# Optimization experiments

Hardware: AMD Instinct MI355X
Metric: run time of the kernel (lower is better)

Reference implementation:

```python
import jax, jax.numpy as jnp
import numpy as np

N = 100_000      # nodes
D = 64           # in_dim
E = 1_600_000    # edges (avg degree 16)
P_L = 0.5        # leaky slope for low-pass gate
P_H = 0.5        # leaky slope for high-pass gate


def setup_inputs() -> dict:
    key = jax.random.key(0)
    ks = jax.random.split(key, 10)
    h = jax.random.normal(ks[0], (N, D), jnp.float32)
    d = jax.random.uniform(ks[1], (N,), jnp.float32)  # degree norms 1/sqrt(deg)
    src = jax.random.randint(ks[2], (E,), 0, N)
    dst = jax.random.randint(ks[3], (E,), 0, N)
    # xavier_normal(gain=1.414) scale ~ gain*sqrt(2/(fan_in+fan_out))
    sg = 1.414 * np.sqrt(2.0 / (2 * D + 1))
    sr = 1.414 * np.sqrt(2.0 / (2 * D + D))
    Wl = jax.random.normal(ks[4], (1, 2 * D), jnp.float32) * sg
    bl = jnp.zeros((1,), jnp.float32)
    Wh = jax.random.normal(ks[5], (1, 2 * D), jnp.float32) * sg
    bh = jnp.zeros((1,), jnp.float32)
    Wr = jax.random.normal(ks[6], (D, 2 * D), jnp.float32) * sr
    br = jnp.zeros((D,), jnp.float32)
    return {"h": h, "d": d, "src": src, "dst": dst,
            "Wl": Wl, "bl": bl, "Wh": Wh, "bh": bh, "Wr": Wr, "br": br}


def reference(h, d, src, dst, Wl, bl, Wh, bh, Wr, br):
    # gate_x(cat([h_dst, h_src])) == h_dst @ W[:, :D] + h_src @ W[:, D:] + b
    # -> project once per node [N], gather per edge [E] (avoids [E,2D] concat)
    low_dst = h @ Wl[0, :D]
    low_src = h @ Wl[0, D:]
    _low = low_dst[dst] + low_src[src] + bl[0]                     # [E]
    g_low = jnp.tanh(jax.nn.relu(jnp.where(_low > 0, _low, -P_L * _low)))

    high_dst = h @ Wh[0, :D]
    high_src = h @ Wh[0, D:]
    _high = high_dst[dst] + high_src[src] + bh[0]                  # [E]
    g_high = jnp.tanh(-jax.nn.relu(jnp.where(_high > 0, _high, -P_H * _high)))

    dd = d[dst] * d[src]                                           # [E]
    e_low = g_low * dd
    e_high = g_high * dd

    h_src = h[src]                                                 # [E, D]
    z_low = jax.ops.segment_sum(h_src * e_low[:, None], dst, num_segments=N)
    z_high = jax.ops.segment_sum(h_src * e_high[:, None], dst, num_segments=N)

    z = jnp.concatenate([z_low, z_high], axis=1)                   # [N, 2D]
    return z @ Wr.T + br                                           # [N, D]
```

## Files before the change

kernel.cpp:

```cpp
#include <hip/hip_runtime.h>
#include <hip/hip_fp16.h>
#include <math.h>

#define N_NODES 100000
#define D_DIM   64
#define N_EDGES 1600000
#define P_L 0.5f
#define P_H 0.5f

#define NPB   32
#define NB    3125
#define TILE  2048
#define NT    784
#define GRP   28
#define GT    28
#define CAP   768
#define ZS    132


typedef unsigned int uint;
typedef unsigned short ushort_t;
typedef float f2 __attribute__((ext_vector_type(2)));

__device__ inline ushort_t f2bf(float f) {
    uint u = __float_as_uint(f);
    uint r = (u + 0x7fffu + ((u >> 16) & 1u)) >> 16;
    return (ushort_t)r;
}

__device__ inline float tanh_pos(float x) {
    return 1.f - 2.f / (__expf(2.f * x) + 1.f);
}

__device__ inline void fma16(uint gy, uint4 hv, f2* acc) {
    float el = __half2float(__ushort_as_half((unsigned short)(gy & 0xffffu)));
    float eh = __half2float(__ushort_as_half((unsigned short)(gy >> 16)));
    f2 f01 = {__uint_as_float(hv.x << 16), __uint_as_float(hv.x & 0xffff0000u)};
    f2 f23 = {__uint_as_float(hv.y << 16), __uint_as_float(hv.y & 0xffff0000u)};
    f2 f45 = {__uint_as_float(hv.z << 16), __uint_as_float(hv.z & 0xffff0000u)};
    f2 f67 = {__uint_as_float(hv.w << 16), __uint_as_float(hv.w & 0xffff0000u)};
    acc[0] += f01 * el; acc[1] += f23 * el; acc[2] += f45 * el; acc[3] += f67 * el;
    acc[4] += f01 * eh; acc[5] += f23 * eh; acc[6] += f45 * eh; acc[7] += f67 * eh;
}

__device__ inline unsigned long long match_dl(int dl, bool active) {
    unsigned long long m = __ballot(active);
    #pragma unroll
    for (int b = 0; b < 5; ++b) {
        unsigned long long bal = __ballot(active && ((dl >> b) & 1));
        m &= ((dl >> b) & 1) ? bal : ~bal;
    }
    return m;
}

__global__ __launch_bounds__(256) void node_gates_kernel(
    const float* __restrict__ h, const float* __restrict__ dvec,
    const float* __restrict__ Wl, const float* __restrict__ Wh,
    ushort_t* __restrict__ hbf,
    float4* __restrict__ gdst4, float4* __restrict__ gsrc4)
{
    int tid = threadIdx.x;
    int lane = tid & 63;
    int half = lane >> 5;
    int l32 = lane & 31;
    int node = blockIdx.x * 8 + (tid >> 6) * 2 + half;

    float2 hv2 = *(const float2*)(h + (size_t)node * 64 + l32 * 2);
    uint pk = (uint)f2bf(hv2.x) | ((uint)f2bf(hv2.y) << 16);
    ((uint*)hbf)[(size_t)node * 32 + l32] = pk;

    float pld = hv2.x * Wl[2 * l32]      + hv2.y * Wl[2 * l32 + 1];
    float pls = hv2.x * Wl[64 + 2 * l32] + hv2.y * Wl[64 + 2 * l32 + 1];
    float phd = hv2.x * Wh[2 * l32]      + hv2.y * Wh[2 * l32 + 1];
    float phs = hv2.x * Wh[64 + 2 * l32] + hv2.y * Wh[64 + 2 * l32 + 1];
    #pragma unroll
    for (int m = 16; m >= 1; m >>= 1) {
        pld += __shfl_xor(pld, m);
        pls += __shfl_xor(pls, m);
        phd += __shfl_xor(phd, m);
        phs += __shfl_xor(phs, m);
    }
    if (l32 == 0) {
        float d = dvec[node];
        gdst4[node] = make_float4(pld, phd, d, 0.f);
        gsrc4[node] = make_float4(pls, phs, d, 0.f);
    }
}

__global__ __launch_bounds__(512) void bucket_hist_kernel(const int* __restrict__ dst,
                                                          int* __restrict__ T) {
    __shared__ int hist[NB];
    int tid = threadIdx.x;
    for (int i = tid; i < NB; i += 512) hist[i] = 0;
    __syncthreads();
    int base = blockIdx.x * TILE;
    #pragma unroll
    for (int j = 0; j < TILE / 512; ++j) {
        int e = base + j * 512 + tid;
        if (e < N_EDGES) atomicAdd(&hist[dst[e] >> 5], 1);
    }
    __syncthreads();
    int* row = T + (size_t)blockIdx.x * NB;
    for (int i = tid; i < NB; i += 512) row[i] = hist[i];
}

__global__ __launch_bounds__(1024) void scanA1_kernel(int* __restrict__ T,
                                                      int* __restrict__ S) {
    int b = blockIdx.x * 1024 + threadIdx.x;
    if (b >= NB) return;
    int g = blockIdx.y;
    int run = 0;
    #pragma unroll
    for (int w = g * GT; w < g * GT + GT; ++w) {
        int idx = w * NB + b;
        int v = T[idx];
        T[idx] = run;
        run += v;
    }
    S[(size_t)g * NB + b] = run;
}

__global__ __launch_bounds__(1024) void scanA2_kernel(int* __restrict__ S,
                                                      int* __restrict__ totG) {
    int b = blockIdx.x * 1024 + threadIdx.x;
    if (b >= NB) return;
    int run = 0;
    #pragma unroll
    for (int g = 0; g < GRP; ++g) {
        int idx = g * NB + b;
        int v = S[idx];
        S[idx] = run;
        run += v;
    }
    totG[b] = run;
}

__global__ __launch_bounds__(1024) void scanB_kernel(const int* __restrict__ totG,
                                                     int* __restrict__ baseG,
                                                     int* __restrict__ bucketoffs,
                                                     const float* __restrict__ Wr,
                                                     float* __restrict__ wrt) {
    int tid = threadIdx.x;
    for (int idx = tid; idx < 64 * 128; idx += 1024) {
        int c = idx >> 7;
        int k = idx & 127;
        wrt[k * 64 + c] = Wr[idx];
    }

    __shared__ int scan_lds[1024];
    int a[4];
    int s = 0;
    #pragma unroll
    for (int i = 0; i < 4; ++i) {
        int b = tid * 4 + i;
        a[i] = (b < NB) ? totG[b] : 0;
        s += a[i];
    }
    scan_lds[tid] = s;
    __syncthreads();
    for (int d = 1; d < 1024; d <<= 1) {
        int v = (tid >= d) ? scan_lds[tid - d] : 0;
        __syncthreads();
        scan_lds[tid] += v;
        __syncthreads();
    }
    int excl = scan_lds[tid] - s;
    int total = scan_lds[1023];
    #pragma unroll
    for (int i = 0; i < 4; ++i) {
        int b = tid * 4 + i;
        if (b < NB) { baseG[b] = excl; bucketoffs[b] = excl; }
        excl += a[i];
    }
    if (tid == 0) bucketoffs[NB] = total;
}

__global__ __launch_bounds__(512) void place_kernel(
    const int* __restrict__ src, const int* __restrict__ dst,
    const int* __restrict__ T, const int* __restrict__ S,
    const int* __restrict__ baseG,
    const float4* __restrict__ gdst4, const float4* __restrict__ gsrc4,
    const float* __restrict__ bl, const float* __restrict__ bh,
    uint2* __restrict__ ebuf)
{
    __shared__ int cur[NB];
    int tid = threadIdx.x;
    const int* row  = T + (size_t)blockIdx.x * NB;
    const int* Srow = S + (size_t)(blockIdx.x / GT) * NB;
    for (int i = tid; i < NB; i += 512) cur[i] = row[i] + Srow[i] + baseG[i];
    __syncthreads();

    float bl0 = bl[0], bh0 = bh[0];
    int base = blockIdx.x * TILE;
    #pragma unroll
    for (int j = 0; j < TILE / 512; ++j) {
        int e = base + j * 512 + tid;
        if (e >= N_EDGES) continue;
        int t = dst[e];
        int s = src[e];
        float4 gt = gdst4[t];
        float4 gs = gsrc4[s];
        float xl = gt.x + gs.x + bl0;
        float xh = gt.y + gs.y + bh0;
        float ll = xl > 0.f ? xl : -P_L * xl;
        float hh = xh > 0.f ? xh : -P_H * xh;
        float dd = gt.z * gs.z;
        float el =  tanh_pos(ll) * dd;
        float eh = -tanh_pos(hh) * dd;
        uint ge = (uint)__half_as_ushort(__float2half_rn(el))
                | ((uint)__half_as_ushort(__float2half_rn(eh)) << 16);
        int b  = t >> 5;
        uint dl = (uint)(t & 31);
        int pos = atomicAdd(&cur[b], 1);
        ebuf[pos] = make_uint2((uint)s | (dl << 17), ge);
    }
}

__global__ __launch_bounds__(512) void accum_final_kernel(
    const int* __restrict__ bucketoffs, const uint2* __restrict__ ebuf,
    const ushort_t* __restrict__ hbf, const float* __restrict__ wrt,
    const float* __restrict__ br, float* __restrict__ out)
{
    __shared__ float z[NPB * ZS];
    __shared__ uint2 srec[CAP];
    __shared__ int ncount[NPB];
    __shared__ int nbase[NPB];
    __shared__ int ncur[NPB];

    int tid = threadIdx.x;
    int lane = tid & 63;
    int bk = blockIdx.x;
    int beg = bucketoffs[bk];
    int end = bucketoffs[bk + 1];
    int cnt = end - beg;
    if (cnt > CAP) cnt = CAP;

    if (tid < NPB) ncount[tid] = 0;

    bool hA = tid < cnt;
    bool hB = tid + 512 < cnt;
    uint2 rA = hA ? ebuf[beg + tid] : make_uint2(0, 0);
    uint2 rB = hB ? ebuf[beg + tid + 512] : make_uint2(0, 0);

    {
        const uint* pa = (const uint*)(hbf + (size_t)(rA.x & 0x1FFFF) * 64);
        const uint* pb = (const uint*)(hbf + (size_t)(rB.x & 0x1FFFF) * 64);
        uint p0 = hA ? pa[0]  : 0u;
        uint p1 = hA ? pa[16] : 0u;
        uint p2 = hB ? pb[0]  : 0u;
        uint p3 = hB ? pb[16] : 0u;
        asm volatile("" :: "v"(p0), "v"(p1), "v"(p2), "v"(p3));
    }
    __syncthreads();

    int dlA = (int)((rA.x >> 17) & 31u);
    int dlB = (int)((rB.x >> 17) & 31u);

    unsigned long long mA = match_dl(dlA, hA);
    if (hA && lane == (int)__builtin_ctzll(mA))
        atomicAdd(&ncount[dlA], (int)__popcll(mA));
    unsigned long long mB = match_dl(dlB, hB);
    if (hB && lane == (int)__builtin_ctzll(mB))
        atomicAdd(&ncount[dlB], (int)__popcll(mB));
    __syncthreads();

    if (tid < 32) {
        int v = ncount[tid];
        int p = v;
        #pragma unroll
        for (int d = 1; d < 32; d <<= 1) {
            int x = __shfl_up(p, d);
            if (tid >= d) p += x;
        }
        nbase[tid] = p - v;
        ncur[tid]  = p - v;
    }
    __syncthreads();

    if (hA) {
        int ldr = (int)__builtin_ctzll(mA);
        int base = 0;
        if (lane == ldr) base = atomicAdd(&ncur[dlA], (int)__popcll(mA));
        base = __shfl(base, ldr);
        int rank = (int)__popcll(mA & ((1ull << lane) - 1ull));
        srec[base + rank] = rA;
    }
    if (hB) {
        int ldr = (int)__builtin_ctzll(mB);
        int base = 0;
        if (lane == ldr) base = atomicAdd(&ncur[dlB], (int)__popcll(mB));
        base = __shfl(base, ldr);
        int rank = (int)__popcll(mB & ((1ull << lane) - 1ull));
        srec[base + rank] = rB;
    }
    __syncthreads();

    int sg = tid >> 3;
    int l8 = tid & 7;
    int node4 = sg >> 1;
    int par = sg & 1;
    int rbeg = nbase[node4];
    int rend = ncur[node4];

    f2 acc[8];
    #pragma unroll
    for (int j = 0; j < 8; ++j) acc[j] = (f2){0.f, 0.f};

    int k = rbeg + par;
    for (; k + 6 < rend; k += 8) {
        uint2 r0 = srec[k];
        uint2 r1 = srec[k + 2];
        uint2 r2 = srec[k + 4];
        uint2 r3 = srec[k + 6];
        uint4 h0 = *(const uint4*)(hbf + (size_t)(r0.x & 0x1FFFF) * 64 + l8 * 8);
        uint4 h1 = *(const uint4*)(hbf + (size_t)(r1.x & 0x1FFFF) * 64 + l8 * 8);
        uint4 h2 = *(const uint4*)(hbf + (size_t)(r2.x & 0x1FFFF) * 64 + l8 * 8);
        uint4 h3 = *(const uint4*)(hbf + (size_t)(r3.x & 0x1FFFF) * 64 + l8 * 8);
        fma16(r0.y, h0, acc);
        fma16(r1.y, h1, acc);
        fma16(r2.y, h2, acc);
        fma16(r3.y, h3, acc);
    }
    for (; k < rend; k += 2) {
        uint2 r0 = srec[k];
        uint4 hv = *(const uint4*)(hbf + (size_t)(r0.x & 0x1FFFF) * 64 + l8 * 8);
        fma16(r0.y, hv, acc);
    }

    float* zp = &z[node4 * ZS + l8 * 8];
    if (par == 0) {
        *(float4*)(zp + 0)  = make_float4(acc[0].x, acc[0].y, acc[1].x, acc[1].y);
        *(float4*)(zp + 4)  = make_float4(acc[2].x, acc[2].y, acc[3].x, acc[3].y);
        *(float4*)(zp + 64) = make_float4(acc[4].x, acc[4].y, acc[5].x, acc[5].y);
        *(float4*)(zp + 68) = make_float4(acc[6].x, acc[6].y, acc[7].x, acc[7].y);
    }
    __syncthreads();
    if (par == 1) {
        float4 z0 = *(float4*)(zp + 0);
        float4 z1 = *(float4*)(zp + 4);
        float4 z2 = *(float4*)(zp + 64);
        float4 z3 = *(float4*)(zp + 68);
        *(float4*)(zp + 0)  = make_float4(z0.x + acc[0].x, z0.y + acc[0].y, z0.z + acc[1].x, z0.w + acc[1].y);
        *(float4*)(zp + 4)  = make_float4(z1.x + acc[2].x, z1.y + acc[2].y, z1.z + acc[3].x, z1.w + acc[3].y);
        *(float4*)(zp + 64) = make_float4(z2.x + acc[4].x, z2.y + acc[4].y, z2.z + acc[5].x, z2.w + acc[5].y);
        *(float4*)(zp + 68) = make_float4(z3.x + acc[6].x, z3.y + acc[6].y, z3.z + acc[7].x, z3.w + acc[7].y);
    }
    __syncthreads();

    int node = tid >> 4;
    int g = tid & 15;
    f2 fa0 = {0.f, 0.f}, fa1 = {0.f, 0.f};
    const float* zrow = z + node * ZS;
    #pragma unroll 2
    for (int kk = 0; kk < 128; kk += 4) {
        float4 z4 = *(const float4*)(zrow + kk);
        const float* wp = wrt + kk * 64 + g * 4;
        float4 w0 = *(const float4*)(wp);
        float4 w1 = *(const float4*)(wp + 64);
        float4 w2 = *(const float4*)(wp + 128);
        float4 w3 = *(const float4*)(wp + 192);
        fa0 += (f2){w0.x, w0.y} * z4.x; fa1 += (f2){w0.z, w0.w} * z4.x;
        fa0 += (f2){w1.x, w1.y} * z4.y; fa1 += (f2){w1.z, w1.w} * z4.y;
        fa0 += (f2){w2.x, w2.y} * z4.z; fa1 += (f2){w2.z, w2.w} * z4.z;
        fa0 += (f2){w3.x, w3.y} * z4.w; fa1 += (f2){w3.z, w3.w} * z4.w;
    }
    int n = bk * NPB + node;
    float* op = out + (size_t)n * 64 + g * 4;
    const float* bp = br + g * 4;
    *(float4*)(op) = make_float4(fa0.x + bp[0], fa0.y + bp[1], fa1.x + bp[2], fa1.y + bp[3]);
}

extern "C" void kernel_launch(void* const* d_in, const int* in_sizes, int n_in,
                              void* d_out, int out_size, void* d_ws, size_t ws_size,
                              hipStream_t stream) {
    const float* h    = (const float*)d_in[0];
    const float* dvec = (const float*)d_in[1];
    const int*   src  = (const int*)  d_in[2];
    const int*   dst  = (const int*)  d_in[3];
    const float* Wl   = (const float*)d_in[4];
    const float* bl   = (const float*)d_in[5];
    const float* Wh   = (const float*)d_in[6];
    const float* bh   = (const float*)d_in[7];
    const float* Wr   = (const float*)d_in[8];
    const float* br   = (const float*)d_in[9];
    float* out = (float*)d_out;

    char* ws = (char*)d_ws;
    size_t off = 0;
    auto alloc = [&](size_t bytes) { char* p = ws + off; off += (bytes + 255) & ~size_t(255); return p; };

    ushort_t* hbf       = (ushort_t*)alloc((size_t)N_NODES * 64 * 2);
    float4*   gdst4     = (float4*)  alloc((size_t)N_NODES * 16);
    float4*   gsrc4     = (float4*)  alloc((size_t)N_NODES * 16);
    float*    wrt       = (float*)   alloc(64 * 128 * 4);
    int*      T         = (int*)     alloc((size_t)NT * NB * 4);
    int*      S         = (int*)     alloc((size_t)GRP * NB * 4);
    int*      totG      = (int*)     alloc((size_t)NB * 4);
    int*      baseG     = (int*)     alloc((size_t)NB * 4);
    int*      bucketoffs= (int*)     alloc((size_t)(NB + 1) * 4);
    uint2*    ebuf      = (uint2*)   alloc((size_t)N_EDGES * 8);

    node_gates_kernel<<<N_NODES / 8, 256, 0, stream>>>(h, dvec, Wl, Wh, hbf, gdst4, gsrc4);
    bucket_hist_kernel<<<NT, 512, 0, stream>>>(dst, T);
    {
        dim3 g1((NB + 1023) / 1024, GRP);
        scanA1_kernel<<<g1, 1024, 0, stream>>>(T, S);
    }
    scanA2_kernel<<<(NB + 1023) / 1024, 1024, 0, stream>>>(S, totG);
    scanB_kernel<<<1, 1024, 0, stream>>>(totG, baseG, bucketoffs, Wr, wrt);
    place_kernel<<<NT, 512, 0, stream>>>(src, dst, T, S, baseG, gdst4, gsrc4, bl, bh, ebuf);
    accum_final_kernel<<<NB, 512, 0, stream>>>(bucketoffs, ebuf, hbf, wrt, br, out);
}
```

Measured before the change: 305.9 us.

## Split each accumulation bucket across two 256-thread blocks by node half

The accumulation kernel now launches two 256-thread blocks per 32-node bucket. Each block reads the whole bucket's edge records but keeps only those whose destination falls in its 16-node half, then sorts, accumulates and projects just those nodes. The aim is more, smaller blocks with less shared memory each, which should help occupancy and load balance. In exchange every bucket's records are read twice, the hbf prefetch touch is dropped, and a new CAPH cap of 512 records per half could truncate edges if a half-bucket holds more.

```diff
diff --git a/kernel.cpp b/kernel.cpp
--- a/kernel.cpp
+++ b/kernel.cpp
@@ -14,7 +14,8 @@
 #define NT    784
 #define GRP   28
 #define GT    28
-#define CAP   768
+#define CAPB  768
+#define CAPH  512
 #define ZS    132
 
 
@@ -43,10 +44,10 @@
     acc[4] += f01 * eh; acc[5] += f23 * eh; acc[6] += f45 * eh; acc[7] += f67 * eh;
 }
 
-__device__ inline unsigned long long match_dl(int dl, bool active) {
+__device__ inline unsigned long long match4(int dl, bool active) {
     unsigned long long m = __ballot(active);
     #pragma unroll
-    for (int b = 0; b < 5; ++b) {
+    for (int b = 0; b < 4; ++b) {
         unsigned long long bal = __ballot(active && ((dl >> b) & 1));
         m &= ((dl >> b) & 1) ? bal : ~bal;
     }
@@ -216,59 +217,60 @@
     }
 }
 
-__global__ __launch_bounds__(512) void accum_final_kernel(
+__global__ __launch_bounds__(256) void accum_final_kernel(
     const int* __restrict__ bucketoffs, const uint2* __restrict__ ebuf,
     const ushort_t* __restrict__ hbf, const float* __restrict__ wrt,
     const float* __restrict__ br, float* __restrict__ out)
 {
-    __shared__ float z[NPB * ZS];
-    __shared__ uint2 srec[CAP];
-    __shared__ int ncount[NPB];
-    __shared__ int nbase[NPB];
-    __shared__ int ncur[NPB];
+    __shared__ float z[16 * ZS];
+    __shared__ uint2 srec[CAPH];
+    __shared__ int ncount[16];
+    __shared__ int nbase[16];
+    __shared__ int ncur[16];
 
     int tid = threadIdx.x;
     int lane = tid & 63;
-    int bk = blockIdx.x;
+    int bk = blockIdx.x >> 1;
+    int hf = blockIdx.x & 1;
     int beg = bucketoffs[bk];
     int end = bucketoffs[bk + 1];
     int cnt = end - beg;
-    if (cnt > CAP) cnt = CAP;
-
-    if (tid < NPB) ncount[tid] = 0;
+    if (cnt > CAPB) cnt = CAPB;
+
+    if (tid < 16) ncount[tid] = 0;
 
     bool hA = tid < cnt;
-    bool hB = tid + 512 < cnt;
-    uint2 rA = hA ? ebuf[beg + tid] : make_uint2(0, 0);
-    uint2 rB = hB ? ebuf[beg + tid + 512] : make_uint2(0, 0);
-
-    {
-        const uint* pa = (const uint*)(hbf + (size_t)(rA.x & 0x1FFFF) * 64);
-        const uint* pb = (const uint*)(hbf + (size_t)(rB.x & 0x1FFFF) * 64);
-        uint p0 = hA ? pa[0]  : 0u;
-        uint p1 = hA ? pa[16] : 0u;
-        uint p2 = hB ? pb[0]  : 0u;
-        uint p3 = hB ? pb[16] : 0u;
-        asm volatile("" :: "v"(p0), "v"(p1), "v"(p2), "v"(p3));
-    }
-    __syncthreads();
-
-    int dlA = (int)((rA.x >> 17) & 31u);
-    int dlB = (int)((rB.x >> 17) & 31u);
-
-    unsigned long long mA = match_dl(dlA, hA);
-    if (hA && lane == (int)__builtin_ctzll(mA))
+    bool hB = tid + 256 < cnt;
+    bool hC = tid + 512 < cnt;
+    uint2 rA = hA ? ebuf[beg + tid]       : make_uint2(0, 0);
+    uint2 rB = hB ? ebuf[beg + tid + 256] : make_uint2(0, 0);
+    uint2 rC = hC ? ebuf[beg + tid + 512] : make_uint2(0, 0);
+    __syncthreads();
+
+    int dA5 = (int)((rA.x >> 17) & 31u);
+    int dB5 = (int)((rB.x >> 17) & 31u);
+    int dC5 = (int)((rC.x >> 17) & 31u);
+    bool oA = hA && ((dA5 >> 4) == hf);
+    bool oB = hB && ((dB5 >> 4) == hf);
+    bool oC = hC && ((dC5 >> 4) == hf);
+    int dlA = dA5 & 15, dlB = dB5 & 15, dlC = dC5 & 15;
+
+    unsigned long long mA = match4(dlA, oA);
+    if (oA && lane == (int)__builtin_ctzll(mA))
         atomicAdd(&ncount[dlA], (int)__popcll(mA));
-    unsigned long long mB = match_dl(dlB, hB);
-    if (hB && lane == (int)__builtin_ctzll(mB))
+    unsigned long long mB = match4(dlB, oB);
+    if (oB && lane == (int)__builtin_ctzll(mB))
         atomicAdd(&ncount[dlB], (int)__popcll(mB));
-    __syncthreads();
-
-    if (tid < 32) {
+    unsigned long long mC = match4(dlC, oC);
+    if (oC && lane == (int)__builtin_ctzll(mC))
+        atomicAdd(&ncount[dlC], (int)__popcll(mC));
+    __syncthreads();
+
+    if (tid < 16) {
         int v = ncount[tid];
         int p = v;
         #pragma unroll
-        for (int d = 1; d < 32; d <<= 1) {
+        for (int d = 1; d < 16; d <<= 1) {
             int x = __shfl_up(p, d);
             if (tid >= d) p += x;
         }
@@ -277,21 +279,29 @@
     }
     __syncthreads();
 
-    if (hA) {
+    if (oA) {
         int ldr = (int)__builtin_ctzll(mA);
         int base = 0;
         if (lane == ldr) base = atomicAdd(&ncur[dlA], (int)__popcll(mA));
         base = __shfl(base, ldr);
-        int rank = (int)__popcll(mA & ((1ull << lane) - 1ull));
-        srec[base + rank] = rA;
-    }
-    if (hB) {
+        int pos = base + (int)__popcll(mA & ((1ull << lane) - 1ull));
+        if (pos < CAPH) srec[pos] = rA;
+    }
+    if (oB) {
         int ldr = (int)__builtin_ctzll(mB);
         int base = 0;
         if (lane == ldr) base = atomicAdd(&ncur[dlB], (int)__popcll(mB));
         base = __shfl(base, ldr);
-        int rank = (int)__popcll(mB & ((1ull << lane) - 1ull));
-        srec[base + rank] = rB;
+        int pos = base + (int)__popcll(mB & ((1ull << lane) - 1ull));
+        if (pos < CAPH) srec[pos] = rB;
+    }
+    if (oC) {
+        int ldr = (int)__builtin_ctzll(mC);
+        int base = 0;
+        if (lane == ldr) base = atomicAdd(&ncur[dlC], (int)__popcll(mC));
+        base = __shfl(base, ldr);
+        int pos = base + (int)__popcll(mC & ((1ull << lane) - 1ull));
+        if (pos < CAPH) srec[pos] = rC;
     }
     __syncthreads();
 
@@ -301,6 +311,7 @@
     int par = sg & 1;
     int rbeg = nbase[node4];
     int rend = ncur[node4];
+    if (rend > CAPH) rend = CAPH;
 
     f2 acc[8];
     #pragma unroll
@@ -364,7 +375,7 @@
         fa0 += (f2){w2.x, w2.y} * z4.z; fa1 += (f2){w2.z, w2.w} * z4.z;
         fa0 += (f2){w3.x, w3.y} * z4.w; fa1 += (f2){w3.z, w3.w} * z4.w;
     }
-    int n = bk * NPB + node;
+    int n = bk * NPB + hf * 16 + node;
     float* op = out + (size_t)n * 64 + g * 4;
     const float* bp = br + g * 4;
     *(float4*)(op) = make_float4(fa0.x + bp[0], fa0.y + bp[1], fa1.x + bp[2], fa1.y + bp[3]);
@@ -409,5 +420,5 @@
     scanA2_kernel<<<(NB + 1023) / 1024, 1024, 0, stream>>>(S, totG);
     scanB_kernel<<<1, 1024, 0, stream>>>(totG, baseG, bucketoffs, Wr, wrt);
     place_kernel<<<NT, 512, 0, stream>>>(src, dst, T, S, baseG, gdst4, gsrc4, bl, bh, ebuf);
-    accum_final_kernel<<<NB, 512, 0, stream>>>(bucketoffs, ebuf, hbf, wrt, br, out);
-}
+    accum_final_kernel<<<NB * 2, 256, 0, stream>>>(bucketoffs, ebuf, hbf, wrt, br, out);
+}
```

Result: faster. 285.4 us (-6.7%).
